# Performance work log

Hardware: AMD Instinct MI355X
Metric: run time of the kernel (lower is better)

Reference implementation:

```python
import jax, jax.numpy as jnp
import numpy as np

B, T, D, H = 64, 2048, 512, 512
NEG_INF = -1e9


def setup_inputs() -> dict:
    key = jax.random.key(0)
    k1, k2, k3 = jax.random.split(key, 3)
    x = jax.random.normal(k1, (B, D), dtype=jnp.float32)
    enc_outs = jax.random.normal(k2, (B, T, D), dtype=jnp.float32)
    # Dense(hidden) applied to concat([x, context]) -> weight [2*D, H]
    W = jax.random.normal(k3, (2 * D, H), dtype=jnp.float32) * (1.0 / np.sqrt(2 * D))
    b = jnp.zeros((H,), dtype=jnp.float32)
    actual_step = 100  # scalar step counter (int state)
    return {"x": x, "enc_outs": enc_outs, "W": W, "b": b, "actual_step": actual_step}


def reference(x, enc_outs, W, b, actual_step):
    # Dot-product attention of query x over enc_outs, masking the current step.
    # scores: [B, T]
    scores = jnp.einsum('bd,btd->bt', x, enc_outs)
    t_idx = jnp.arange(enc_outs.shape[1])
    scores = jnp.where((t_idx == actual_step)[None, :], NEG_INF, scores)
    alignment = jax.nn.softmax(scores, axis=-1)          # [B, T]
    context = jnp.einsum('bt,btd->bd', alignment, enc_outs)  # [B, D]
    # gate = sigmoid(Dense(concat([x, context])))
    att = jax.nn.sigmoid(jnp.concatenate([x, context], axis=-1) @ W + b)  # [B, H]
    content_selected = att * x                           # requires H == D
    return content_selected
```

## Files before the change

kernel.cpp:

```cpp
#include <hip/hip_runtime.h>
#include <math.h>

#define BB 64
#define TT 2048
#define DD 512
#define HH 512
#define NC 32
#define CHUNK (TT / NC)
#define TH 8.0f

__global__ __launch_bounds__(256) void k1_partial(
    const float* __restrict__ x, const float* __restrict__ enc,
    const int* __restrict__ step_ptr,
    float* __restrict__ ws_m, float* __restrict__ ws_l, float* __restrict__ ws_c)
{
    const int chunk = blockIdx.x;
    const int b     = blockIdx.y;
    const int tid   = threadIdx.x;
    const int w     = tid >> 6;
    const int lane  = tid & 63;
    const int step  = *step_ptr;
    const int t0    = chunk * CHUNK;

    const float4* xr = (const float4*)(x + (size_t)b * DD);
    const float4 xa = xr[lane];
    const float4 xb = xr[64 + lane];

    float m = -1e30f, l = 0.f;
    float4 ca = make_float4(0.f, 0.f, 0.f, 0.f);
    float4 cb = make_float4(0.f, 0.f, 0.f, 0.f);

    const float4* er = (const float4*)(enc + (size_t)b * TT * DD);

    #pragma unroll 4
    for (int i = w; i < CHUNK; i += 4) {
        const int t = t0 + i;
        const float4* row = er + (size_t)t * (DD / 4);
        const float4 ea = row[lane];
        const float4 eb = row[64 + lane];

        float s = ea.x * xa.x + ea.y * xa.y + ea.z * xa.z + ea.w * xa.w
                + eb.x * xb.x + eb.y * xb.y + eb.z * xb.z + eb.w * xb.w;
        #pragma unroll
        for (int off = 32; off; off >>= 1) s += __shfl_xor(s, off, 64);

        if (t != step) {
            float wgt;
            if (s > m + TH) {
                const float sc = __expf(m - s);
                l *= sc;
                ca.x *= sc; ca.y *= sc; ca.z *= sc; ca.w *= sc;
                cb.x *= sc; cb.y *= sc; cb.z *= sc; cb.w *= sc;
                m = s;
                wgt = 1.f;
            } else {
                wgt = __expf(s - m);
            }
            l += wgt;
            ca.x = fmaf(wgt, ea.x, ca.x);
            ca.y = fmaf(wgt, ea.y, ca.y);
            ca.z = fmaf(wgt, ea.z, ca.z);
            ca.w = fmaf(wgt, ea.w, ca.w);
            cb.x = fmaf(wgt, eb.x, cb.x);
            cb.y = fmaf(wgt, eb.y, cb.y);
            cb.z = fmaf(wgt, eb.z, cb.z);
            cb.w = fmaf(wgt, eb.w, cb.w);
        }
    }

    __shared__ float ls_m[4], ls_l[4];
    __shared__ float ls_c[4][DD];
    if (lane == 0) { ls_m[w] = m; ls_l[w] = l; }
    {
        float* cw = ls_c[w];
        const int d0 = lane * 4;
        cw[d0 + 0] = ca.x; cw[d0 + 1] = ca.y; cw[d0 + 2] = ca.z; cw[d0 + 3] = ca.w;
        cw[256 + d0 + 0] = cb.x; cw[256 + d0 + 1] = cb.y;
        cw[256 + d0 + 2] = cb.z; cw[256 + d0 + 3] = cb.w;
    }
    __syncthreads();

    const float M = fmaxf(fmaxf(ls_m[0], ls_m[1]), fmaxf(ls_m[2], ls_m[3]));
    const float f0 = __expf(ls_m[0] - M);
    const float f1 = __expf(ls_m[1] - M);
    const float f2 = __expf(ls_m[2] - M);
    const float f3 = __expf(ls_m[3] - M);
    const float L = ls_l[0] * f0 + ls_l[1] * f1 + ls_l[2] * f2 + ls_l[3] * f3;

    const int bc = b * NC + chunk;
    for (int d = tid; d < DD; d += 256) {
        const float v = ls_c[0][d] * f0 + ls_c[1][d] * f1
                      + ls_c[2][d] * f2 + ls_c[3][d] * f3;
        ws_c[(size_t)bc * DD + d] = v;
    }
    if (tid == 0) { ws_m[bc] = M; ws_l[bc] = L; }
}

__global__ __launch_bounds__(256) void k2_gemm(
    const float* __restrict__ x, const float* __restrict__ W,
    const float* __restrict__ bias,
    const float* __restrict__ ws_m, const float* __restrict__ ws_l,
    const float* __restrict__ ws_c,
    float* __restrict__ out)
{
    const int g   = blockIdx.x;
    const int b   = blockIdx.y;
    const int tid = threadIdx.x;

    __shared__ float concat[2 * DD];
    __shared__ float fac[NC];
    __shared__ float4 part[256];

    float M = -1e30f;
    #pragma unroll
    for (int i = 0; i < NC; ++i) M = fmaxf(M, ws_m[b * NC + i]);
    float L = 0.f;
    #pragma unroll
    for (int i = 0; i < NC; ++i) L += ws_l[b * NC + i] * __expf(ws_m[b * NC + i] - M);
    const float invL = 1.f / L;
    if (tid < NC) fac[tid] = __expf(ws_m[b * NC + tid] - M);
    __syncthreads();

    for (int d = tid; d < DD; d += 256) {
        concat[d] = x[(size_t)b * DD + d];
        float acc = 0.f;
        #pragma unroll 8
        for (int i = 0; i < NC; ++i)
            acc = fmaf(ws_c[(size_t)(b * NC + i) * DD + d], fac[i], acc);
        concat[DD + d] = acc * invL;
    }
    __syncthreads();

    const int cl   = tid & 15;
    const int kq   = tid >> 4;
    const int col4 = g * 16 + cl;
    const float4* W4 = (const float4*)W;

    float4 acc = make_float4(0.f, 0.f, 0.f, 0.f);
    const int kbase = kq * 64;
    #pragma unroll 8
    for (int kk = 0; kk < 64; ++kk) {
        const int k = kbase + kk;
        const float4 wv = W4[(size_t)k * (HH / 4) + col4];
        const float cv = concat[k];
        acc.x = fmaf(cv, wv.x, acc.x);
        acc.y = fmaf(cv, wv.y, acc.y);
        acc.z = fmaf(cv, wv.z, acc.z);
        acc.w = fmaf(cv, wv.w, acc.w);
    }
    part[tid] = acc;
    __syncthreads();

    #pragma unroll
    for (int s = 8; s; s >>= 1) {
        if (kq < s) {
            const float4 o = part[(kq + s) * 16 + cl];
            acc.x += o.x; acc.y += o.y; acc.z += o.z; acc.w += o.w;
            part[tid] = acc;
        }
        __syncthreads();
    }

    if (kq == 0) {
        const int h = col4 * 4;
        const float4 bv = *(const float4*)(bias + h);
        const float4 xv = *(const float4*)(concat + h);
        float4 r;
        r.x = xv.x / (1.f + __expf(-(acc.x + bv.x)));
        r.y = xv.y / (1.f + __expf(-(acc.y + bv.y)));
        r.z = xv.z / (1.f + __expf(-(acc.z + bv.z)));
        r.w = xv.w / (1.f + __expf(-(acc.w + bv.w)));
        *(float4*)(out + (size_t)b * DD + h) = r;
    }
}

extern "C" void kernel_launch(void* const* d_in, const int* in_sizes, int n_in,
                              void* d_out, int out_size, void* d_ws, size_t ws_size,
                              hipStream_t stream) {
    const float* x    = (const float*)d_in[0];
    const float* enc  = (const float*)d_in[1];
    const float* W    = (const float*)d_in[2];
    const float* bias = (const float*)d_in[3];
    const int*   step = (const int*)d_in[4];
    float* out = (float*)d_out;
    float* ws  = (float*)d_ws;

    float* ws_m = ws;
    float* ws_l = ws + (size_t)BB * NC;
    float* ws_c = ws + (size_t)2 * BB * NC;

    dim3 g1(NC, BB), blk(256);
    k1_partial<<<g1, blk, 0, stream>>>(x, enc, step, ws_m, ws_l, ws_c);

    dim3 g2(8, BB);
    k2_gemm<<<g2, blk, 0, stream>>>(x, W, bias, ws_m, ws_l, ws_c, out);
}
```

Before: 60.64 us.

## Batch attention rows with prefetch, split merge kernel, batch-tiled gate GEMM

The partial-attention kernel now gives each wave 16 contiguous rows, processed four at a time with double-buffered register prefetch and a single rescale check per group. The context merge moves into its own small kernel. The gate GEMM is restructured so each block handles 8 batch rows, reusing every W load across them instead of rereading W per batch row. The cost is an extra kernel launch and a ctx round trip through global memory.

```diff
diff --git a/kernel.cpp b/kernel.cpp
--- a/kernel.cpp
+++ b/kernel.cpp
@@ -20,51 +20,73 @@
     const int w     = tid >> 6;
     const int lane  = tid & 63;
     const int step  = *step_ptr;
-    const int t0    = chunk * CHUNK;
+    const int trow0 = chunk * CHUNK + w * 16;
 
     const float4* xr = (const float4*)(x + (size_t)b * DD);
     const float4 xa = xr[lane];
     const float4 xb = xr[64 + lane];
 
+    const float4* __restrict__ rp =
+        (const float4*)(enc + (size_t)b * TT * DD) + (size_t)trow0 * 128 + lane;
+
     float m = -1e30f, l = 0.f;
-    float4 ca = make_float4(0.f, 0.f, 0.f, 0.f);
-    float4 cb = make_float4(0.f, 0.f, 0.f, 0.f);
-
-    const float4* er = (const float4*)(enc + (size_t)b * TT * DD);
-
-    #pragma unroll 4
-    for (int i = w; i < CHUNK; i += 4) {
-        const int t = t0 + i;
-        const float4* row = er + (size_t)t * (DD / 4);
-        const float4 ea = row[lane];
-        const float4 eb = row[64 + lane];
-
-        float s = ea.x * xa.x + ea.y * xa.y + ea.z * xa.z + ea.w * xa.w
-                + eb.x * xb.x + eb.y * xb.y + eb.z * xb.z + eb.w * xb.w;
-        #pragma unroll
-        for (int off = 32; off; off >>= 1) s += __shfl_xor(s, off, 64);
-
-        if (t != step) {
-            float wgt;
-            if (s > m + TH) {
-                const float sc = __expf(m - s);
-                l *= sc;
-                ca.x *= sc; ca.y *= sc; ca.z *= sc; ca.w *= sc;
-                cb.x *= sc; cb.y *= sc; cb.z *= sc; cb.w *= sc;
-                m = s;
-                wgt = 1.f;
-            } else {
-                wgt = __expf(s - m);
+    float4 ca = make_float4(0.f,0.f,0.f,0.f), cb = make_float4(0.f,0.f,0.f,0.f);
+
+    float4 A[2][4], Bv[2][4];
+    #pragma unroll
+    for (int k = 0; k < 4; ++k) {
+        A[0][k]  = rp[k * 128];
+        Bv[0][k] = rp[k * 128 + 64];
+    }
+
+    #pragma unroll
+    for (int j = 0; j < 4; ++j) {
+        const int cur = j & 1, nx = cur ^ 1;
+        if (j < 3) {
+            #pragma unroll
+            for (int k = 0; k < 4; ++k) {
+                A[nx][k]  = rp[((j + 1) * 4 + k) * 128];
+                Bv[nx][k] = rp[((j + 1) * 4 + k) * 128 + 64];
             }
-            l += wgt;
-            ca.x = fmaf(wgt, ea.x, ca.x);
-            ca.y = fmaf(wgt, ea.y, ca.y);
-            ca.z = fmaf(wgt, ea.z, ca.z);
-            ca.w = fmaf(wgt, ea.w, ca.w);
-            cb.x = fmaf(wgt, eb.x, cb.x);
-            cb.y = fmaf(wgt, eb.y, cb.y);
-            cb.z = fmaf(wgt, eb.z, cb.z);
-            cb.w = fmaf(wgt, eb.w, cb.w);
+        }
+        float s[4];
+        #pragma unroll
+        for (int k = 0; k < 4; ++k) {
+            const float4 ea = A[cur][k], eb = Bv[cur][k];
+            s[k] = ea.x*xa.x + ea.y*xa.y + ea.z*xa.z + ea.w*xa.w
+                 + eb.x*xb.x + eb.y*xb.y + eb.z*xb.z + eb.w*xb.w;
+        }
+        #pragma unroll
+        for (int off = 32; off; off >>= 1) {
+            #pragma unroll
+            for (int k = 0; k < 4; ++k) s[k] += __shfl_xor(s[k], off, 64);
+        }
+        #pragma unroll
+        for (int k = 0; k < 4; ++k)
+            if (trow0 + j * 4 + k == step) s[k] = -1e30f;
+
+        const float bm = fmaxf(fmaxf(s[0], s[1]), fmaxf(s[2], s[3]));
+        if (bm > m + TH) {
+            const float sc = __expf(m - bm);
+            l *= sc;
+            ca.x *= sc; ca.y *= sc; ca.z *= sc; ca.w *= sc;
+            cb.x *= sc; cb.y *= sc; cb.z *= sc; cb.w *= sc;
+            m = bm;
+        }
+        float wk[4];
+        #pragma unroll
+        for (int k = 0; k < 4; ++k) wk[k] = __expf(s[k] - m);
+        l += (wk[0] + wk[1]) + (wk[2] + wk[3]);
+        #pragma unroll
+        for (int k = 0; k < 4; ++k) {
+            ca.x = fmaf(wk[k], A[cur][k].x, ca.x);
+            ca.y = fmaf(wk[k], A[cur][k].y, ca.y);
+            ca.z = fmaf(wk[k], A[cur][k].z, ca.z);
+            ca.w = fmaf(wk[k], A[cur][k].w, ca.w);
+            cb.x = fmaf(wk[k], Bv[cur][k].x, cb.x);
+            cb.y = fmaf(wk[k], Bv[cur][k].y, cb.y);
+            cb.z = fmaf(wk[k], Bv[cur][k].z, cb.z);
+            cb.w = fmaf(wk[k], Bv[cur][k].w, cb.w);
         }
     }
 
@@ -96,20 +118,13 @@
     if (tid == 0) { ws_m[bc] = M; ws_l[bc] = L; }
 }
 
-__global__ __launch_bounds__(256) void k2_gemm(
-    const float* __restrict__ x, const float* __restrict__ W,
-    const float* __restrict__ bias,
+__global__ __launch_bounds__(256) void k1b_merge(
     const float* __restrict__ ws_m, const float* __restrict__ ws_l,
-    const float* __restrict__ ws_c,
-    float* __restrict__ out)
+    const float* __restrict__ ws_c, float* __restrict__ ctx)
 {
-    const int g   = blockIdx.x;
-    const int b   = blockIdx.y;
+    const int b = blockIdx.x;
     const int tid = threadIdx.x;
-
-    __shared__ float concat[2 * DD];
     __shared__ float fac[NC];
-    __shared__ float4 part[256];
 
     float M = -1e30f;
     #pragma unroll
@@ -117,60 +132,117 @@
     float L = 0.f;
     #pragma unroll
     for (int i = 0; i < NC; ++i) L += ws_l[b * NC + i] * __expf(ws_m[b * NC + i] - M);
-    const float invL = 1.f / L;
-    if (tid < NC) fac[tid] = __expf(ws_m[b * NC + tid] - M);
-    __syncthreads();
-
+    const float inv = 1.f / L;
+    if (tid < NC) fac[tid] = __expf(ws_m[b * NC + tid] - M) * inv;
+    __syncthreads();
+
+    #pragma unroll
     for (int d = tid; d < DD; d += 256) {
-        concat[d] = x[(size_t)b * DD + d];
         float acc = 0.f;
         #pragma unroll 8
         for (int i = 0; i < NC; ++i)
             acc = fmaf(ws_c[(size_t)(b * NC + i) * DD + d], fac[i], acc);
-        concat[DD + d] = acc * invL;
-    }
-    __syncthreads();
-
-    const int cl   = tid & 15;
-    const int kq   = tid >> 4;
-    const int col4 = g * 16 + cl;
-    const float4* W4 = (const float4*)W;
-
-    float4 acc = make_float4(0.f, 0.f, 0.f, 0.f);
-    const int kbase = kq * 64;
-    #pragma unroll 8
-    for (int kk = 0; kk < 64; ++kk) {
-        const int k = kbase + kk;
-        const float4 wv = W4[(size_t)k * (HH / 4) + col4];
-        const float cv = concat[k];
-        acc.x = fmaf(cv, wv.x, acc.x);
-        acc.y = fmaf(cv, wv.y, acc.y);
-        acc.z = fmaf(cv, wv.z, acc.z);
-        acc.w = fmaf(cv, wv.w, acc.w);
-    }
-    part[tid] = acc;
-    __syncthreads();
-
-    #pragma unroll
-    for (int s = 8; s; s >>= 1) {
-        if (kq < s) {
-            const float4 o = part[(kq + s) * 16 + cl];
-            acc.x += o.x; acc.y += o.y; acc.z += o.z; acc.w += o.w;
-            part[tid] = acc;
-        }
-        __syncthreads();
-    }
-
-    if (kq == 0) {
-        const int h = col4 * 4;
-        const float4 bv = *(const float4*)(bias + h);
-        const float4 xv = *(const float4*)(concat + h);
-        float4 r;
-        r.x = xv.x / (1.f + __expf(-(acc.x + bv.x)));
-        r.y = xv.y / (1.f + __expf(-(acc.y + bv.y)));
-        r.z = xv.z / (1.f + __expf(-(acc.z + bv.z)));
-        r.w = xv.w / (1.f + __expf(-(acc.w + bv.w)));
-        *(float4*)(out + (size_t)b * DD + h) = r;
+        ctx[(size_t)b * DD + d] = acc;
+    }
+}
+
+#define COLS 8
+__device__ __forceinline__ int cidx(int k, int bb) {
+    return (k >> 5) * 260 + (k & 31) * 8 + bb;
+}
+
+__global__ __launch_bounds__(256) void k2_gemm(
+    const float* __restrict__ x, const float* __restrict__ ctx,
+    const float* __restrict__ W, const float* __restrict__ bias,
+    float* __restrict__ out)
+{
+    const int g   = blockIdx.x;
+    const int bg  = blockIdx.y;
+    const int tid = threadIdx.x;
+
+    __shared__ float  con[32 * 260];
+    __shared__ float4 part[4][COLS][8];
+
+    const float4* x4 = (const float4*)x;
+    const float4* c4 = (const float4*)ctx;
+
+    for (int idx = tid; idx < 2048; idx += 256) {
+        const int bb = idx >> 8, k4 = idx & 255;
+        const int b  = bg * 8 + bb;
+        const float4 v = (k4 < 128) ? x4[(size_t)b * 128 + k4]
+                                    : c4[(size_t)b * 128 + (k4 - 128)];
+        const int k = k4 * 4;
+        con[cidx(k + 0, bb)] = v.x;
+        con[cidx(k + 1, bb)] = v.y;
+        con[cidx(k + 2, bb)] = v.z;
+        con[cidx(k + 3, bb)] = v.w;
+    }
+    __syncthreads();
+
+    const int cl   = tid & 7;
+    const int kseg = tid >> 3;
+    const int col4 = g * COLS + cl;
+    const float4* Wp = (const float4*)W + (size_t)(kseg * 32) * 128 + col4;
+
+    float4 acc[8];
+    #pragma unroll
+    for (int bb = 0; bb < 8; ++bb) acc[bb] = make_float4(0.f,0.f,0.f,0.f);
+
+    #pragma unroll 4
+    for (int kk = 0; kk < 32; ++kk) {
+        const float4 wv = Wp[(size_t)kk * 128];
+        const int k = kseg * 32 + kk;
+        const float4 c0 = *(const float4*)&con[cidx(k, 0)];
+        const float4 c1 = *(const float4*)&con[cidx(k, 4)];
+        const float cv[8] = {c0.x, c0.y, c0.z, c0.w, c1.x, c1.y, c1.z, c1.w};
+        #pragma unroll
+        for (int bb = 0; bb < 8; ++bb) {
+            acc[bb].x = fmaf(cv[bb], wv.x, acc[bb].x);
+            acc[bb].y = fmaf(cv[bb], wv.y, acc[bb].y);
+            acc[bb].z = fmaf(cv[bb], wv.z, acc[bb].z);
+            acc[bb].w = fmaf(cv[bb], wv.w, acc[bb].w);
+        }
+    }
+
+    #pragma unroll
+    for (int off = 8; off <= 32; off <<= 1) {
+        #pragma unroll
+        for (int bb = 0; bb < 8; ++bb) {
+            acc[bb].x += __shfl_xor(acc[bb].x, off, 64);
+            acc[bb].y += __shfl_xor(acc[bb].y, off, 64);
+            acc[bb].z += __shfl_xor(acc[bb].z, off, 64);
+            acc[bb].w += __shfl_xor(acc[bb].w, off, 64);
+        }
+    }
+    const int wv_ = tid >> 6, lane = tid & 63;
+    if (lane < 8) {
+        #pragma unroll
+        for (int bb = 0; bb < 8; ++bb) part[wv_][lane][bb] = acc[bb];
+    }
+    __syncthreads();
+
+    if (tid < 64) {
+        const int bb = tid >> 3, cl2 = tid & 7;
+        float4 r = part[0][cl2][bb];
+        #pragma unroll
+        for (int ww = 1; ww < 4; ++ww) {
+            const float4 p = part[ww][cl2][bb];
+            r.x += p.x; r.y += p.y; r.z += p.z; r.w += p.w;
+        }
+        const int c4i = g * COLS + cl2;
+        const int h   = c4i * 4;
+        const int b   = bg * 8 + bb;
+        const float4 bv = ((const float4*)bias)[c4i];
+        const float xv0 = con[cidx(h + 0, bb)];
+        const float xv1 = con[cidx(h + 1, bb)];
+        const float xv2 = con[cidx(h + 2, bb)];
+        const float xv3 = con[cidx(h + 3, bb)];
+        float4 o;
+        o.x = xv0 / (1.f + __expf(-(r.x + bv.x)));
+        o.y = xv1 / (1.f + __expf(-(r.y + bv.y)));
+        o.z = xv2 / (1.f + __expf(-(r.z + bv.z)));
+        o.w = xv3 / (1.f + __expf(-(r.w + bv.w)));
+        ((float4*)out)[(size_t)b * 128 + c4i] = o;
     }
 }
 
@@ -186,12 +258,11 @@
     float* ws  = (float*)d_ws;
 
     float* ws_m = ws;
-    float* ws_l = ws + (size_t)BB * NC;
-    float* ws_c = ws + (size_t)2 * BB * NC;
-
-    dim3 g1(NC, BB), blk(256);
-    k1_partial<<<g1, blk, 0, stream>>>(x, enc, step, ws_m, ws_l, ws_c);
-
-    dim3 g2(8, BB);
-    k2_gemm<<<g2, blk, 0, stream>>>(x, W, bias, ws_m, ws_l, ws_c, out);
-}
+    float* ws_l = ws_m + (size_t)BB * NC;
+    float* ws_c = ws_l + (size_t)BB * NC;
+    float* ctx  = ws_c + (size_t)BB * NC * DD;
+
+    k1_partial<<<dim3(NC, BB), 256, 0, stream>>>(x, enc, step, ws_m, ws_l, ws_c);
+    k1b_merge<<<dim3(BB), 256, 0, stream>>>(ws_m, ws_l, ws_c, ctx);
+    k2_gemm<<<dim3(16, 8), 256, 0, stream>>>(x, ctx, W, bias, out);
+}
```

Result: no change. 60.94 us (+0.5%).
